# Optimization experiments

Measured on AMD Instinct MI355X. Metric: run time of the kernel, lower is better.

Reference implementation:

```python
import jax, jax.numpy as jnp
import numpy as np

B_TRUE, S, HEADS, DIM_HEAD, DIM, N = 2, 2, 8, 64, 512, 1024
BS = B_TRUE * S            # effective batch = (b s)
DIM_INNER = HEADS * DIM_HEAD
ALL_HEADS = S * HEADS
EPS = 1e-5


def setup_inputs() -> dict:
    key = jax.random.key(0)
    ks = jax.random.split(key, 8)
    inv = 0.02
    x = jax.random.normal(ks[0], (BS, N, DIM), dtype=jnp.float32)
    mask = jax.random.randint(ks[1], (BS, N), 0, 2).astype(bool)
    gamma = jnp.ones((DIM,), dtype=jnp.float32)
    w_qkv = jax.random.normal(ks[2], (3 * DIM_INNER, DIM), dtype=jnp.float32) * inv
    w_gates = jax.random.normal(ks[3], (HEADS, DIM), dtype=jnp.float32) * inv
    b_gates = jnp.zeros((HEADS,), dtype=jnp.float32)
    w_pre = jax.random.normal(ks[4], (ALL_HEADS, ALL_HEADS), dtype=jnp.float32) * 0.25
    w_post = jax.random.normal(ks[5], (ALL_HEADS, ALL_HEADS), dtype=jnp.float32) * 0.25
    w_out = jax.random.normal(ks[6], (DIM, DIM_INNER), dtype=jnp.float32) * inv
    return {"x": x, "mask": mask, "gamma": gamma, "w_qkv": w_qkv,
            "w_gates": w_gates, "b_gates": b_gates, "w_pre": w_pre,
            "w_post": w_post, "w_out": w_out}


def _rmsnorm(x, gamma):
    # einn.Norm('b... [d]', mean=False, bias=False): RMSNorm over last dim
    var = jnp.mean(jnp.square(x), axis=-1, keepdims=True)
    return x * jax.lax.rsqrt(var + EPS) * gamma


def reference(x, mask, gamma, w_qkv, w_gates, b_gates, w_pre, w_post, w_out):
    bs, n, dim = x.shape
    b = bs // S
    x = _rmsnorm(x, gamma)

    # QKV: 'b n (qkv h d) -> qkv b h n d'
    qkv = jnp.einsum('bnd,ed->bne', x, w_qkv)
    qkv = qkv.reshape(bs, n, 3, HEADS, DIM_HEAD).transpose(2, 0, 3, 1, 4)
    q, k, v = qkv[0], qkv[1], qkv[2]
    q = q * (DIM_HEAD ** 0.5)  # NOTE: source MULTIPLIES by sqrt(dim_head)

    sim = jnp.einsum('bhid,bhjd->bhij', q, k)  # [bs, h, n, n]
    mask_value = -jnp.finfo(sim.dtype).max

    # pre talking-heads: 1x1 conv across (s h) channels
    sim = sim.reshape(b, ALL_HEADS, n, n)
    sim = jnp.einsum('oi,binm->bonm', w_pre, sim).reshape(bs, HEADS, n, n)

    # padding mask over keys j
    sim = jnp.where(mask[:, None, None, :], sim, mask_value)

    # causal mask
    causal = jnp.triu(jnp.ones((n, n), dtype=bool), 1)
    sim = jnp.where(causal, mask_value, sim)

    attn = jax.nn.softmax(sim, axis=-1)
    post_softmax_attn = attn

    # post talking-heads
    attn = attn.reshape(b, ALL_HEADS, n, n)
    attn = jnp.einsum('oi,binm->bonm', w_post, attn).reshape(bs, HEADS, n, n)

    out = jnp.einsum('bhij,bhjd->bhid', attn, v)  # [bs, h, n, d]

    # sigmoid gates from normed x: 'b n h -> b h n 1'
    gates = jax.nn.sigmoid(jnp.einsum('bnd,hd->bnh', x, w_gates) + b_gates)
    out = out * gates.transpose(0, 2, 1)[..., None]

    # 'b h n d -> b n (h d)' then Linear(dim_inner, dim, bias=False)
    out = out.transpose(0, 2, 1, 3).reshape(bs, n, DIM_INNER)
    out = jnp.einsum('bne,de->bnd', out, w_out)
    return (out, post_softmax_attn)
```

## Files before the change

kernel.cpp:

```cpp
#include <hip/hip_runtime.h>
#include <cfloat>
#include <math.h>

#define B2   2
#define BS4  4
#define NH   8
#define DH   64
#define DIM  512
#define NSEQ 1024
#define AH   16

typedef __attribute__((ext_vector_type(8))) short short8;
typedef __attribute__((ext_vector_type(4))) float floatx4;
typedef __attribute__((ext_vector_type(2))) float float2v;

__device__ inline unsigned short f2bf(float x) {
    unsigned int u = __float_as_uint(x);
    unsigned int r = (u + 0x7fffu + ((u >> 16) & 1u)) >> 16;
    return (unsigned short)r;
}
__device__ inline float bf2f(unsigned short h) {
    return __uint_as_float(((unsigned int)h) << 16);
}
__device__ inline void split2(float x, unsigned short& h, unsigned short& l) {
    h = f2bf(x);
    l = f2bf(x - bf2f(h));
}

__device__ inline float2v pk_fma(float2v a, float2v b, float2v c) {
#if __has_builtin(__builtin_elementwise_fma)
    return __builtin_elementwise_fma(a, b, c);
#else
    float2v r;
    r[0] = fmaf(a[0], b[0], c[0]);
    r[1] = fmaf(a[1], b[1], c[1]);
    return r;
#endif
}

template<int MT, int NT_, bool SPLIT>
__device__ inline void mfma_nt_core(
    const unsigned short* __restrict__ Ah, const unsigned short* __restrict__ Al,
    const unsigned short* __restrict__ Bh, const unsigned short* __restrict__ Bl,
    int K, int lda, int ldb, int arow, int bcol, floatx4 acc[MT][NT_])
{
    int lane = threadIdx.x & 63;
    int lr = lane & 15, lq = lane >> 4;
    for (int k0 = 0; k0 < K; k0 += 32) {
        short8 ah[MT], al[MT], bh[NT_], bl[NT_];
        #pragma unroll
        for (int mi = 0; mi < MT; ++mi) {
            size_t off = (size_t)(arow + mi * 16 + lr) * lda + k0 + lq * 8;
            ah[mi] = *(const short8*)(Ah + off);
            if (SPLIT) al[mi] = *(const short8*)(Al + off);
        }
        #pragma unroll
        for (int ni = 0; ni < NT_; ++ni) {
            size_t off = (size_t)(bcol + ni * 16 + lr) * ldb + k0 + lq * 8;
            bh[ni] = *(const short8*)(Bh + off);
            if (SPLIT) bl[ni] = *(const short8*)(Bl + off);
        }
        #pragma unroll
        for (int mi = 0; mi < MT; ++mi)
            #pragma unroll
            for (int ni = 0; ni < NT_; ++ni) {
                acc[mi][ni] = __builtin_amdgcn_mfma_f32_16x16x32_bf16(ah[mi], bh[ni], acc[mi][ni], 0, 0, 0);
                if (SPLIT) {
                    acc[mi][ni] = __builtin_amdgcn_mfma_f32_16x16x32_bf16(ah[mi], bl[ni], acc[mi][ni], 0, 0, 0);
                    acc[mi][ni] = __builtin_amdgcn_mfma_f32_16x16x32_bf16(al[mi], bh[ni], acc[mi][ni], 0, 0, 0);
                }
            }
    }
}

__global__ __launch_bounds__(256) void k_rmsnorm_gates(
    const float* __restrict__ x, const float* __restrict__ gamma,
    const float* __restrict__ wg, const float* __restrict__ bg,
    unsigned short* __restrict__ xn_h, unsigned short* __restrict__ xn_l,
    float* __restrict__ gates)
{
    int r = blockIdx.x;
    int tid = threadIdx.x;
    const float* xr = x + (size_t)r * DIM;
    float v0 = xr[tid];
    float v1 = xr[tid + 256];
    float ss = v0 * v0 + v1 * v1;
    #pragma unroll
    for (int off = 32; off > 0; off >>= 1) ss += __shfl_down(ss, off, 64);
    __shared__ float sc[4];
    __shared__ float scw[NH][4];
    if ((tid & 63) == 0) sc[tid >> 6] = ss;
    __syncthreads();
    float tot = sc[0] + sc[1] + sc[2] + sc[3];
    float rs = rsqrtf(tot * (1.0f / DIM) + 1e-5f);
    float n0 = v0 * rs * gamma[tid];
    float n1 = v1 * rs * gamma[tid + 256];
    unsigned short hh, ll;
    split2(n0, hh, ll);
    xn_h[(size_t)r * DIM + tid] = hh; xn_l[(size_t)r * DIM + tid] = ll;
    split2(n1, hh, ll);
    xn_h[(size_t)r * DIM + tid + 256] = hh; xn_l[(size_t)r * DIM + tid + 256] = ll;
    #pragma unroll
    for (int h = 0; h < NH; ++h) {
        float p = n0 * wg[h * DIM + tid] + n1 * wg[h * DIM + tid + 256];
        #pragma unroll
        for (int off = 32; off > 0; off >>= 1) p += __shfl_down(p, off, 64);
        if ((tid & 63) == 0) scw[h][tid >> 6] = p;
    }
    __syncthreads();
    if (tid < NH) {
        float g = scw[tid][0] + scw[tid][1] + scw[tid][2] + scw[tid][3] + bg[tid];
        gates[(size_t)r * NH + tid] = 1.0f / (1.0f + __expf(-g));
    }
}

#define NQKV (3 * DIM * NH * DH)
#define NOUT (DIM * NH * DH)
__global__ __launch_bounds__(256) void k_cvt(
    const float* __restrict__ wqkv, const float* __restrict__ wout,
    unsigned short* __restrict__ wq_h, unsigned short* __restrict__ wq_l,
    unsigned short* __restrict__ wout_b)
{
    for (int i = blockIdx.x * 256 + threadIdx.x; i < NQKV + NOUT; i += gridDim.x * 256) {
        if (i < NQKV) {
            unsigned short hh, ll;
            split2(wqkv[i], hh, ll);
            wq_h[i] = hh; wq_l[i] = ll;
        } else {
            wout_b[i - NQKV] = f2bf(wout[i - NQKV]);
        }
    }
}

__global__ __launch_bounds__(64) void k_qkv_mfma(
    const unsigned short* __restrict__ xn_h, const unsigned short* __restrict__ xn_l,
    const unsigned short* __restrict__ wq_h, const unsigned short* __restrict__ wq_l,
    unsigned short* __restrict__ q_h, unsigned short* __restrict__ q_l,
    unsigned short* __restrict__ k_h, unsigned short* __restrict__ k_l,
    unsigned short* __restrict__ vT_b)
{
    __shared__ unsigned short vs[64][68];
    int bx = blockIdx.x;
    int am = blockIdx.y * 64;
    int bn = bx * 64;
    floatx4 acc[4][4];
    #pragma unroll
    for (int mi = 0; mi < 4; ++mi)
        #pragma unroll
        for (int ni = 0; ni < 4; ++ni) acc[mi][ni] = (floatx4){0.f, 0.f, 0.f, 0.f};
    mfma_nt_core<4, 4, true>(xn_h, xn_l, wq_h, wq_l, DIM, DIM, DIM, am, bn, acc);
    int tid = threadIdx.x;
    int lane = tid & 63, lr = lane & 15, lq = lane >> 4;

    if (bx < 16) {
        const bool isq = (bx < 8);
        unsigned short* dh = isq ? q_h : k_h;
        unsigned short* dl = isq ? q_l : k_l;
        const float scale = isq ? 8.0f : 1.0f;
        #pragma unroll
        for (int mi = 0; mi < 4; ++mi)
            #pragma unroll
            for (int ni = 0; ni < 4; ++ni)
                #pragma unroll
                for (int r = 0; r < 4; ++r) {
                    int row = am + mi * 16 + lq * 4 + r;
                    int col = bn + ni * 16 + lr;
                    int bs = row >> 10, npos = row & 1023;
                    int h = (col >> 6) & 7, d = col & 63;
                    size_t idx = (((size_t)(bs * 8 + h)) * NSEQ + npos) * DH + d;
                    unsigned short hh, ll;
                    split2(acc[mi][ni][r] * scale, hh, ll);
                    dh[idx] = hh; dl[idx] = ll;
                }
    } else {
        const int h = bx - 16;
        const int bs = (blockIdx.y * 64) >> 10;
        const int bh = bs * 8 + h;
        const int npos_base = (blockIdx.y * 64) & 1023;
        #pragma unroll
        for (int mi = 0; mi < 4; ++mi)
            #pragma unroll
            for (int ni = 0; ni < 4; ++ni)
                #pragma unroll
                for (int r = 0; r < 4; ++r) {
                    int nl  = mi * 16 + lq * 4 + r;
                    int dl2 = ni * 16 + lr;
                    vs[dl2][nl] = f2bf(acc[mi][ni][r]);
                }
        __syncthreads();
        #pragma unroll
        for (int it = 0; it < 8; ++it) {
            int d = it * 8 + (tid >> 3);
            int c8 = (tid & 7) * 8;
            unsigned short* dst = vT_b + ((size_t)bh * DH + d) * NSEQ + npos_base + c8;
            *(ulonglong2*)dst = *(ulonglong2*)&vs[d][c8];
        }
    }
}

__global__ __launch_bounds__(64) void k_qk_mfma(
    const unsigned short* __restrict__ q_h, const unsigned short* __restrict__ q_l,
    const unsigned short* __restrict__ k_h, const unsigned short* __restrict__ k_l,
    float* __restrict__ sim_ws)
{
    __shared__ float cs[64][68];
    int am0 = blockIdx.y * 64;
    int bn0 = blockIdx.x * 64;
    if (bn0 > am0 + 63) return;
    int bh = blockIdx.z;
    int b_true = bh >> 4;
    int c = ((bh >> 3) & 1) * 8 + (bh & 7);
    const unsigned short* Ah = q_h + (size_t)bh * NSEQ * DH;
    const unsigned short* Al = q_l + (size_t)bh * NSEQ * DH;
    const unsigned short* Bh = k_h + (size_t)bh * NSEQ * DH;
    const unsigned short* Bl = k_l + (size_t)bh * NSEQ * DH;
    floatx4 acc[4][4];
    #pragma unroll
    for (int mi = 0; mi < 4; ++mi)
        #pragma unroll
        for (int ni = 0; ni < 4; ++ni) acc[mi][ni] = (floatx4){0.f, 0.f, 0.f, 0.f};
    mfma_nt_core<4, 4, true>(Ah, Al, Bh, Bl, DH, DH, DH, am0, bn0, acc);

    int tid = threadIdx.x;
    int lane = tid & 63, lr = lane & 15, lq = lane >> 4;
    #pragma unroll
    for (int mi = 0; mi < 4; ++mi)
        #pragma unroll
        for (int ni = 0; ni < 4; ++ni)
            #pragma unroll
            for (int r = 0; r < 4; ++r) {
                int lrow = mi * 16 + lq * 4 + r;
                int lcol = ni * 16 + lr;
                cs[lrow][lcol] = acc[mi][ni][r];
            }
    __syncthreads();
    int trow = tid >> 4;
    int tcol = (tid & 15) * 4;
    #pragma unroll
    for (int it = 0; it < 16; ++it) {
        int row = it * 4 + trow;
        float4 v4 = *(float4*)&cs[row][tcol];
        size_t gaddr = ((size_t)(b_true * NSEQ + am0 + row) * 16 + c) * NSEQ + bn0 + tcol;
        *(float4*)(sim_ws + gaddr) = v4;
    }
}

__global__ __launch_bounds__(256) void k_talk(
    float* __restrict__ sim_ws, const int* __restrict__ mask,
    const float* __restrict__ wpre, const float* __restrict__ wpost,
    float* __restrict__ probs_out)
{
    const int i = blockIdx.x;
    const int b = blockIdx.y;
    const int tid = threadIdx.x;
    const int wid = tid >> 6, lane = tid & 63;
    const int j0 = tid << 2;
    const size_t cstride = (size_t)NSEQ * NSEQ;
    float* simrow = sim_ws + (size_t)(b * NSEQ + i) * (16 * NSEQ);

    const int4 mi0 = *(const int4*)(mask + (size_t)(b * 2 + 0) * NSEQ + j0);
    const int4 mi1 = *(const int4*)(mask + (size_t)(b * 2 + 1) * NSEQ + j0);
    bool mb[2][4];
    mb[0][0] = (mi0.x != 0) && (j0 + 0 <= i);
    mb[0][1] = (mi0.y != 0) && (j0 + 1 <= i);
    mb[0][2] = (mi0.z != 0) && (j0 + 2 <= i);
    mb[0][3] = (mi0.w != 0) && (j0 + 3 <= i);
    mb[1][0] = (mi1.x != 0) && (j0 + 0 <= i);
    mb[1][1] = (mi1.y != 0) && (j0 + 1 <= i);
    mb[1][2] = (mi1.z != 0) && (j0 + 2 <= i);
    mb[1][3] = (mi1.w != 0) && (j0 + 3 <= i);

    float2v val[16][2];
    #pragma unroll
    for (int o = 0; o < 16; ++o) {
        val[o][0] = (float2v){0.f, 0.f};
        val[o][1] = (float2v){0.f, 0.f};
    }
    #pragma unroll
    for (int c = 0; c < 16; ++c) {
        float4 r = *(const float4*)(simrow + c * NSEQ + j0);
        float2v r01 = (float2v){r.x, r.y};
        float2v r23 = (float2v){r.z, r.w};
        #pragma unroll
        for (int o = 0; o < 16; ++o) {
            float w = wpre[o * 16 + c];
            float2v wv = (float2v){w, w};
            val[o][0] = pk_fma(wv, r01, val[o][0]);
            val[o][1] = pk_fma(wv, r23, val[o][1]);
        }
    }
    #pragma unroll
    for (int o = 0; o < 16; ++o) {
        const int s = o >> 3;
        if (!mb[s][0]) val[o][0][0] = -FLT_MAX;
        if (!mb[s][1]) val[o][0][1] = -FLT_MAX;
        if (!mb[s][2]) val[o][1][0] = -FLT_MAX;
        if (!mb[s][3]) val[o][1][1] = -FLT_MAX;
    }

    __shared__ float red[16][4];
    __shared__ float finmx[16];
    __shared__ float fininv[16];

    #pragma unroll
    for (int o = 0; o < 16; ++o) {
        float m = fmaxf(fmaxf(val[o][0][0], val[o][0][1]), fmaxf(val[o][1][0], val[o][1][1]));
        #pragma unroll
        for (int off = 32; off > 0; off >>= 1) m = fmaxf(m, __shfl_xor(m, off, 64));
        if (lane == 0) red[o][wid] = m;
    }
    __syncthreads();
    if (tid < 16)
        finmx[tid] = fmaxf(fmaxf(red[tid][0], red[tid][1]), fmaxf(red[tid][2], red[tid][3]));
    __syncthreads();

    #pragma unroll
    for (int o = 0; o < 16; ++o) {
        float mx = finmx[o];
        float e0 = __expf(val[o][0][0] - mx);
        float e1 = __expf(val[o][0][1] - mx);
        float e2 = __expf(val[o][1][0] - mx);
        float e3 = __expf(val[o][1][1] - mx);
        val[o][0][0] = e0; val[o][0][1] = e1;
        val[o][1][0] = e2; val[o][1][1] = e3;
        float s = (e0 + e1) + (e2 + e3);
        #pragma unroll
        for (int off = 32; off > 0; off >>= 1) s += __shfl_xor(s, off, 64);
        if (lane == 0) red[o][wid] = s;
    }
    __syncthreads();
    if (tid < 16)
        fininv[tid] = 1.0f / (red[tid][0] + red[tid][1] + red[tid][2] + red[tid][3]);
    __syncthreads();

    #pragma unroll
    for (int o = 0; o < 16; ++o) {
        float inv = fininv[o];
        float2v invv = (float2v){inv, inv};
        val[o][0] *= invv;
        val[o][1] *= invv;
        floatx4 st = {val[o][0][0], val[o][0][1], val[o][1][0], val[o][1][1]};
        __builtin_nontemporal_store(st,
            (floatx4*)(probs_out + (size_t)(b * 16 + o) * cstride + (size_t)i * NSEQ + j0));
    }

    unsigned short* a2row = (unsigned short*)simrow;
    #pragma unroll
    for (int o = 0; o < 16; ++o) {
        float2v a01 = (float2v){0.f, 0.f};
        float2v a23 = (float2v){0.f, 0.f};
        #pragma unroll
        for (int c = 0; c < 16; ++c) {
            float w = wpost[o * 16 + c];
            float2v wv = (float2v){w, w};
            a01 = pk_fma(wv, val[c][0], a01);
            a23 = pk_fma(wv, val[c][1], a23);
        }
        unsigned long long pk = (unsigned long long)f2bf(a01[0])
                              | ((unsigned long long)f2bf(a01[1]) << 16)
                              | ((unsigned long long)f2bf(a23[0]) << 32)
                              | ((unsigned long long)f2bf(a23[1]) << 48);
        *(unsigned long long*)(a2row + o * NSEQ + j0) = pk;
    }
}

__global__ __launch_bounds__(64) void k_av_mfma(
    const unsigned short* __restrict__ attn2_il, const unsigned short* __restrict__ vT_b,
    const float* __restrict__ gates, unsigned short* __restrict__ gated_b)
{
    int bh = blockIdx.y;
    int bs = bh >> 3, h = bh & 7;
    int b_true = bh >> 4;
    int c = ((bh >> 3) & 1) * 8 + (bh & 7);
    int am = blockIdx.x * 64;
    const unsigned short* Ah = attn2_il + (size_t)b_true * NSEQ * 32768 + (size_t)c * NSEQ;
    const unsigned short* Bh = vT_b + (size_t)bh * DH * NSEQ;
    floatx4 acc[4][4];
    #pragma unroll
    for (int mi = 0; mi < 4; ++mi)
        #pragma unroll
        for (int ni = 0; ni < 4; ++ni) acc[mi][ni] = (floatx4){0.f, 0.f, 0.f, 0.f};
    mfma_nt_core<4, 4, false>(Ah, nullptr, Bh, nullptr, NSEQ, 32768, NSEQ, am, 0, acc);
    int lane = threadIdx.x & 63, lr = lane & 15, lq = lane >> 4;
    #pragma unroll
    for (int mi = 0; mi < 4; ++mi)
        #pragma unroll
        for (int ni = 0; ni < 4; ++ni)
            #pragma unroll
            for (int r = 0; r < 4; ++r) {
                int i = am + mi * 16 + lq * 4 + r;
                int d = ni * 16 + lr;
                float g = gates[((size_t)bs * NSEQ + i) * NH + h];
                gated_b[((size_t)bs * NSEQ + i) * DIM + h * DH + d] = f2bf(acc[mi][ni][r] * g);
            }
}

__global__ __launch_bounds__(64) void k_out_mfma(
    const unsigned short* __restrict__ gated_b, const unsigned short* __restrict__ wout_b,
    float* __restrict__ out)
{
    int am = blockIdx.y * 64;
    int bn = blockIdx.x * 64;
    floatx4 acc[4][4];
    #pragma unroll
    for (int mi = 0; mi < 4; ++mi)
        #pragma unroll
        for (int ni = 0; ni < 4; ++ni) acc[mi][ni] = (floatx4){0.f, 0.f, 0.f, 0.f};
    mfma_nt_core<4, 4, false>(gated_b, nullptr, wout_b, nullptr, DIM, DIM, DIM, am, bn, acc);
    int lane = threadIdx.x & 63, lr = lane & 15, lq = lane >> 4;
    #pragma unroll
    for (int mi = 0; mi < 4; ++mi)
        #pragma unroll
        for (int ni = 0; ni < 4; ++ni)
            #pragma unroll
            for (int r = 0; r < 4; ++r) {
                int row = am + mi * 16 + lq * 4 + r;
                int col = bn + ni * 16 + lr;
                out[(size_t)row * DIM + col] = acc[mi][ni][r];
            }
}

extern "C" void kernel_launch(void* const* d_in, const int* in_sizes, int n_in,
                              void* d_out, int out_size, void* d_ws, size_t ws_size,
                              hipStream_t stream)
{
    (void)in_sizes; (void)n_in; (void)out_size; (void)ws_size;

    const float* x     = (const float*)d_in[0];
    const int*   mask  = (const int*)  d_in[1];
    const float* gamma = (const float*)d_in[2];
    const float* wqkv  = (const float*)d_in[3];
    const float* wg    = (const float*)d_in[4];
    const float* bg    = (const float*)d_in[5];
    const float* wpre  = (const float*)d_in[6];
    const float* wpost = (const float*)d_in[7];
    const float* wout  = (const float*)d_in[8];

    float* out       = (float*)d_out;
    float* probs_out = out + (size_t)BS4 * NSEQ * DIM;

    char* ws = (char*)d_ws;
    unsigned short* xn_h    = (unsigned short*)(ws);
    unsigned short* xn_l    = (unsigned short*)(ws + 4194304);
    unsigned short* wq_h    = (unsigned short*)(ws + 8388608);
    unsigned short* wq_l    = (unsigned short*)(ws + 9961472);
    unsigned short* wout_b  = (unsigned short*)(ws + 11534336);
    float*          gates   = (float*)         (ws + 12058624);
    unsigned short* q_h     = (unsigned short*)(ws + 12189696);
    unsigned short* q_l     = (unsigned short*)(ws + 16384000);
    unsigned short* k_h     = (unsigned short*)(ws + 20578304);
    unsigned short* k_l     = (unsigned short*)(ws + 24772608);
    unsigned short* vT_b    = (unsigned short*)(ws + 28966912);
    unsigned short* gated_b = (unsigned short*)(ws + 33161216);
    float*          sim_ws  = (float*)         (ws + 37355520);

    k_rmsnorm_gates<<<dim3(BS4 * NSEQ), dim3(256), 0, stream>>>(x, gamma, wg, bg, xn_h, xn_l, gates);
    k_cvt<<<dim3(1024), dim3(256), 0, stream>>>(wqkv, wout, wq_h, wq_l, wout_b);
    k_qkv_mfma<<<dim3(24, 64), dim3(64), 0, stream>>>(xn_h, xn_l, wq_h, wq_l, q_h, q_l, k_h, k_l, vT_b);
    k_qk_mfma<<<dim3(16, 16, 32), dim3(64), 0, stream>>>(q_h, q_l, k_h, k_l, sim_ws);
    k_talk<<<dim3(NSEQ, B2), dim3(256), 0, stream>>>(sim_ws, mask, wpre, wpost, probs_out);
    k_av_mfma<<<dim3(16, 32), dim3(64), 0, stream>>>((unsigned short*)sim_ws, vT_b, gates, gated_b);
    k_out_mfma<<<dim3(8, 64), dim3(64), 0, stream>>>(gated_b, wout_b, out);
}
```

Baseline: 373.4 us.

## Interleave bf16 hi/lo split operands in 8-element chunks for MFMA loads

```diff
diff --git a/kernel.cpp b/kernel.cpp
--- a/kernel.cpp
+++ b/kernel.cpp
@@ -26,6 +26,7 @@
     h = f2bf(x);
     l = f2bf(x - bf2f(h));
 }
+__device__ inline int il_addr(int k) { return ((k >> 3) << 4) + (k & 7); }
 
 __device__ inline float2v pk_fma(float2v a, float2v b, float2v c) {
 #if __has_builtin(__builtin_elementwise_fma)
@@ -38,7 +39,7 @@
 #endif
 }
 
-template<int MT, int NT_, bool SPLIT>
+template<int MT, int NT_, bool SPLIT, bool IL>
 __device__ inline void mfma_nt_core(
     const unsigned short* __restrict__ Ah, const unsigned short* __restrict__ Al,
     const unsigned short* __restrict__ Bh, const unsigned short* __restrict__ Bl,
@@ -47,16 +48,17 @@
     int lane = threadIdx.x & 63;
     int lr = lane & 15, lq = lane >> 4;
     for (int k0 = 0; k0 < K; k0 += 32) {
+        const int ka = IL ? (k0 + lq * 8) * 2 : (k0 + lq * 8);
         short8 ah[MT], al[MT], bh[NT_], bl[NT_];
         #pragma unroll
         for (int mi = 0; mi < MT; ++mi) {
-            size_t off = (size_t)(arow + mi * 16 + lr) * lda + k0 + lq * 8;
+            size_t off = (size_t)(arow + mi * 16 + lr) * lda + ka;
             ah[mi] = *(const short8*)(Ah + off);
             if (SPLIT) al[mi] = *(const short8*)(Al + off);
         }
         #pragma unroll
         for (int ni = 0; ni < NT_; ++ni) {
-            size_t off = (size_t)(bcol + ni * 16 + lr) * ldb + k0 + lq * 8;
+            size_t off = (size_t)(bcol + ni * 16 + lr) * ldb + ka;
             bh[ni] = *(const short8*)(Bh + off);
             if (SPLIT) bl[ni] = *(const short8*)(Bl + off);
         }
@@ -76,8 +78,7 @@
 __global__ __launch_bounds__(256) void k_rmsnorm_gates(
     const float* __restrict__ x, const float* __restrict__ gamma,
     const float* __restrict__ wg, const float* __restrict__ bg,
-    unsigned short* __restrict__ xn_h, unsigned short* __restrict__ xn_l,
-    float* __restrict__ gates)
+    unsigned short* __restrict__ xn_il, float* __restrict__ gates)
 {
     int r = blockIdx.x;
     int tid = threadIdx.x;
@@ -95,11 +96,14 @@
     float rs = rsqrtf(tot * (1.0f / DIM) + 1e-5f);
     float n0 = v0 * rs * gamma[tid];
     float n1 = v1 * rs * gamma[tid + 256];
+    size_t rb = (size_t)r * (2 * DIM);
     unsigned short hh, ll;
     split2(n0, hh, ll);
-    xn_h[(size_t)r * DIM + tid] = hh; xn_l[(size_t)r * DIM + tid] = ll;
+    int a0 = il_addr(tid);
+    xn_il[rb + a0] = hh; xn_il[rb + a0 + 8] = ll;
     split2(n1, hh, ll);
-    xn_h[(size_t)r * DIM + tid + 256] = hh; xn_l[(size_t)r * DIM + tid + 256] = ll;
+    int a1 = il_addr(tid + 256);
+    xn_il[rb + a1] = hh; xn_il[rb + a1 + 8] = ll;
     #pragma unroll
     for (int h = 0; h < NH; ++h) {
         float p = n0 * wg[h * DIM + tid] + n1 * wg[h * DIM + tid + 256];
@@ -118,14 +122,15 @@
 #define NOUT (DIM * NH * DH)
 __global__ __launch_bounds__(256) void k_cvt(
     const float* __restrict__ wqkv, const float* __restrict__ wout,
-    unsigned short* __restrict__ wq_h, unsigned short* __restrict__ wq_l,
-    unsigned short* __restrict__ wout_b)
+    unsigned short* __restrict__ wq_il, unsigned short* __restrict__ wout_b)
 {
     for (int i = blockIdx.x * 256 + threadIdx.x; i < NQKV + NOUT; i += gridDim.x * 256) {
         if (i < NQKV) {
             unsigned short hh, ll;
             split2(wqkv[i], hh, ll);
-            wq_h[i] = hh; wq_l[i] = ll;
+            int e = i >> 9, k = i & 511;
+            size_t a = (size_t)e * (2 * DIM) + il_addr(k);
+            wq_il[a] = hh; wq_il[a + 8] = ll;
         } else {
             wout_b[i - NQKV] = f2bf(wout[i - NQKV]);
         }
@@ -133,10 +138,8 @@
 }
 
 __global__ __launch_bounds__(64) void k_qkv_mfma(
-    const unsigned short* __restrict__ xn_h, const unsigned short* __restrict__ xn_l,
-    const unsigned short* __restrict__ wq_h, const unsigned short* __restrict__ wq_l,
-    unsigned short* __restrict__ q_h, unsigned short* __restrict__ q_l,
-    unsigned short* __restrict__ k_h, unsigned short* __restrict__ k_l,
+    const unsigned short* __restrict__ xn_il, const unsigned short* __restrict__ wq_il,
+    unsigned short* __restrict__ q_il, unsigned short* __restrict__ k_il,
     unsigned short* __restrict__ vT_b)
 {
     __shared__ unsigned short vs[64][68];
@@ -148,14 +151,14 @@
     for (int mi = 0; mi < 4; ++mi)
         #pragma unroll
         for (int ni = 0; ni < 4; ++ni) acc[mi][ni] = (floatx4){0.f, 0.f, 0.f, 0.f};
-    mfma_nt_core<4, 4, true>(xn_h, xn_l, wq_h, wq_l, DIM, DIM, DIM, am, bn, acc);
+    mfma_nt_core<4, 4, true, true>(xn_il, xn_il + 8, wq_il, wq_il + 8,
+                                   DIM, 2 * DIM, 2 * DIM, am, bn, acc);
     int tid = threadIdx.x;
     int lane = tid & 63, lr = lane & 15, lq = lane >> 4;
 
     if (bx < 16) {
         const bool isq = (bx < 8);
-        unsigned short* dh = isq ? q_h : k_h;
-        unsigned short* dl = isq ? q_l : k_l;
+        unsigned short* dst = isq ? q_il : k_il;
         const float scale = isq ? 8.0f : 1.0f;
         #pragma unroll
         for (int mi = 0; mi < 4; ++mi)
@@ -167,10 +170,10 @@
                     int col = bn + ni * 16 + lr;
                     int bs = row >> 10, npos = row & 1023;
                     int h = (col >> 6) & 7, d = col & 63;
-                    size_t idx = (((size_t)(bs * 8 + h)) * NSEQ + npos) * DH + d;
+                    size_t base = (((size_t)(bs * 8 + h)) * NSEQ + npos) * (2 * DH) + il_addr(d);
                     unsigned short hh, ll;
                     split2(acc[mi][ni][r] * scale, hh, ll);
-                    dh[idx] = hh; dl[idx] = ll;
+                    dst[base] = hh; dst[base + 8] = ll;
                 }
     } else {
         const int h = bx - 16;
@@ -199,8 +202,7 @@
 }
 
 __global__ __launch_bounds__(64) void k_qk_mfma(
-    const unsigned short* __restrict__ q_h, const unsigned short* __restrict__ q_l,
-    const unsigned short* __restrict__ k_h, const unsigned short* __restrict__ k_l,
+    const unsigned short* __restrict__ q_il, const unsigned short* __restrict__ k_il,
     float* __restrict__ sim_ws)
 {
     __shared__ float cs[64][68];
@@ -210,16 +212,14 @@
     int bh = blockIdx.z;
     int b_true = bh >> 4;
     int c = ((bh >> 3) & 1) * 8 + (bh & 7);
-    const unsigned short* Ah = q_h + (size_t)bh * NSEQ * DH;
-    const unsigned short* Al = q_l + (size_t)bh * NSEQ * DH;
-    const unsigned short* Bh = k_h + (size_t)bh * NSEQ * DH;
-    const unsigned short* Bl = k_l + (size_t)bh * NSEQ * DH;
+    const unsigned short* A = q_il + (size_t)bh * NSEQ * (2 * DH);
+    const unsigned short* B = k_il + (size_t)bh * NSEQ * (2 * DH);
     floatx4 acc[4][4];
     #pragma unroll
     for (int mi = 0; mi < 4; ++mi)
         #pragma unroll
         for (int ni = 0; ni < 4; ++ni) acc[mi][ni] = (floatx4){0.f, 0.f, 0.f, 0.f};
-    mfma_nt_core<4, 4, true>(Ah, Al, Bh, Bl, DH, DH, DH, am0, bn0, acc);
+    mfma_nt_core<4, 4, true, true>(A, A + 8, B, B + 8, DH, 2 * DH, 2 * DH, am0, bn0, acc);
 
     int tid = threadIdx.x;
     int lane = tid & 63, lr = lane & 15, lq = lane >> 4;
@@ -380,7 +380,7 @@
     for (int mi = 0; mi < 4; ++mi)
         #pragma unroll
         for (int ni = 0; ni < 4; ++ni) acc[mi][ni] = (floatx4){0.f, 0.f, 0.f, 0.f};
-    mfma_nt_core<4, 4, false>(Ah, nullptr, Bh, nullptr, NSEQ, 32768, NSEQ, am, 0, acc);
+    mfma_nt_core<4, 4, false, false>(Ah, nullptr, Bh, nullptr, NSEQ, 32768, NSEQ, am, 0, acc);
     int lane = threadIdx.x & 63, lr = lane & 15, lq = lane >> 4;
     #pragma unroll
     for (int mi = 0; mi < 4; ++mi)
@@ -406,7 +406,7 @@
     for (int mi = 0; mi < 4; ++mi)
         #pragma unroll
         for (int ni = 0; ni < 4; ++ni) acc[mi][ni] = (floatx4){0.f, 0.f, 0.f, 0.f};
-    mfma_nt_core<4, 4, false>(gated_b, nullptr, wout_b, nullptr, DIM, DIM, DIM, am, bn, acc);
+    mfma_nt_core<4, 4, false, false>(gated_b, nullptr, wout_b, nullptr, DIM, DIM, DIM, am, bn, acc);
     int lane = threadIdx.x & 63, lr = lane & 15, lq = lane >> 4;
     #pragma unroll
     for (int mi = 0; mi < 4; ++mi)
@@ -440,24 +440,20 @@
     float* probs_out = out + (size_t)BS4 * NSEQ * DIM;
 
     char* ws = (char*)d_ws;
-    unsigned short* xn_h    = (unsigned short*)(ws);
-    unsigned short* xn_l    = (unsigned short*)(ws + 4194304);
-    unsigned short* wq_h    = (unsigned short*)(ws + 8388608);
-    unsigned short* wq_l    = (unsigned short*)(ws + 9961472);
+    unsigned short* xn_il   = (unsigned short*)(ws);
+    unsigned short* wq_il   = (unsigned short*)(ws + 8388608);
     unsigned short* wout_b  = (unsigned short*)(ws + 11534336);
     float*          gates   = (float*)         (ws + 12058624);
-    unsigned short* q_h     = (unsigned short*)(ws + 12189696);
-    unsigned short* q_l     = (unsigned short*)(ws + 16384000);
-    unsigned short* k_h     = (unsigned short*)(ws + 20578304);
-    unsigned short* k_l     = (unsigned short*)(ws + 24772608);
+    unsigned short* q_il    = (unsigned short*)(ws + 12189696);
+    unsigned short* k_il    = (unsigned short*)(ws + 20578304);
     unsigned short* vT_b    = (unsigned short*)(ws + 28966912);
     unsigned short* gated_b = (unsigned short*)(ws + 33161216);
     float*          sim_ws  = (float*)         (ws + 37355520);
 
-    k_rmsnorm_gates<<<dim3(BS4 * NSEQ), dim3(256), 0, stream>>>(x, gamma, wg, bg, xn_h, xn_l, gates);
-    k_cvt<<<dim3(1024), dim3(256), 0, stream>>>(wqkv, wout, wq_h, wq_l, wout_b);
-    k_qkv_mfma<<<dim3(24, 64), dim3(64), 0, stream>>>(xn_h, xn_l, wq_h, wq_l, q_h, q_l, k_h, k_l, vT_b);
-    k_qk_mfma<<<dim3(16, 16, 32), dim3(64), 0, stream>>>(q_h, q_l, k_h, k_l, sim_ws);
+    k_rmsnorm_gates<<<dim3(BS4 * NSEQ), dim3(256), 0, stream>>>(x, gamma, wg, bg, xn_il, gates);
+    k_cvt<<<dim3(1024), dim3(256), 0, stream>>>(wqkv, wout, wq_il, wout_b);
+    k_qkv_mfma<<<dim3(24, 64), dim3(64), 0, stream>>>(xn_il, wq_il, q_il, k_il, vT_b);
+    k_qk_mfma<<<dim3(16, 16, 32), dim3(64), 0, stream>>>(q_il, k_il, sim_ws);
     k_talk<<<dim3(NSEQ, B2), dim3(256), 0, stream>>>(sim_ws, mask, wpre, wpost, probs_out);
     k_av_mfma<<<dim3(16, 32), dim3(64), 0, stream>>>((unsigned short*)sim_ws, vT_b, gates, gated_b);
     k_out_mfma<<<dim3(8, 64), dim3(64), 0, stream>>>(gated_b, wout_b, out);
```

Result: no change. 373.2 us (-0.1%).
